# Kernel optimization log

Hardware: AMD Instinct MI355X
Metric: run time of the kernel (lower is better)

The kernel has to match this reference:

```python
import jax, jax.numpy as jnp
import numpy as np

TAU = 0.75

def normalize_W(W):
    n = jnp.linalg.norm(W)
    n = jax.nn.relu(n - 1.0) + 1.0
    return W / n

def setup_inputs() -> dict:
    key = jax.random.key(0)
    ks = jax.random.split(key, 14)
    C_in, C_out, K = 64, 128, 3
    B, L = 32, 4096
    nh = 64
    chunk_in_d = C_out * K            # 384
    D = C_in * (K + 2 * (C_out // C_in))  # 448
    r = lambda k, shp, s=1.0: jax.random.normal(k, shp, dtype=jnp.float32) * s
    W = normalize_W(r(ks[4], (D, 32)))
    return {
        "x": r(ks[0], (B, C_in, L)),
        "conv_weight": r(ks[1], (C_out, C_in, K), 0.1),
        "bias_param": r(ks[2], (C_out,), 0.1),
        "grads": r(ks[3], (C_out * C_in * K,), 0.1),
        "W": W,
        "ctrl_w": r(ks[5], (nh, chunk_in_d), 0.05),
        "ctrl_b": r(ks[6], (nh,), 0.05),
        "cw_w": r(ks[7], (K, nh), 0.05),
        "cw_b": r(ks[8], (K,), 0.05),
        "cb_w": r(ks[9], (C_out // C_in, nh), 0.05),
        "cb_b": r(ks[10], (C_out // C_in,), 0.05),
        "cf_w": r(ks[11], (C_out // C_in, nh), 0.05),
        "cf_b": r(ks[12], (C_out // C_in,), 0.05),
        "trigger": 1,
    }

def fw_chunks(grads, W, ctrl_w, ctrl_b, cw_w, cw_b, cb_w, cb_b, cf_w, cf_b, trigger, n_chunks):
    g = grads.reshape(n_chunks, -1)                    # (C_in, C_out*K)
    rep = jax.nn.silu(g @ ctrl_w.T + ctrl_b)           # (C_in, nh)
    w = rep @ cw_w.T + cw_b                            # (C_in, K)
    b = rep @ cb_w.T + cb_b                            # (C_in, C_out/C_in)
    f = rep @ cf_w.T + cf_b                            # (C_in, C_out/C_in)
    q = jnp.concatenate([w.ravel(), b.ravel(), f.ravel()])  # (D,)  first call: no q_ema
    W_upd = W
    if trigger == 1:  # codebook attention / top-k / scatter-EMA path
        dim = w.shape[0]
        att = jax.nn.softmax(q @ W / 0.5)              # (32,)
        v, idx = jax.lax.top_k(att, 2)
        ww = W[:, idx]                                 # (D, 2)
        old_w = ww @ idx.astype(jnp.float32)[:, None]  # (D, 1) -- indices used as weights, as in source
        s_att = jnp.zeros((att.shape[0],), jnp.float32).at[idx].set(v)
        W_contrib = old_w @ s_att[None, :]             # (D, 32)
        mask = jnp.ones(W.shape, jnp.float32).at[:, idx].set(TAU)
        W_upd = normalize_W(mask * W + (1.0 - mask) * W_contrib)
        nw, nb, nf = w.shape[1], b.shape[1], f.shape[1]
        o_w = old_w[: nw * dim]
        o_b = old_w[nw * dim : (nw + nb) * dim]
        o_f = old_w[-nf * dim :]
        w = TAU * w + (1.0 - TAU) * o_w.reshape(w.shape)
        b = TAU * b + (1.0 - TAU) * o_b.reshape(b.shape)
        f = TAU * f + (1.0 - TAU) * o_f.reshape(f.shape)
    f = f.reshape(-1)[None, :, None]                   # (1, C_out, 1)
    return w[None], b.reshape(-1), f, W_upd

def reference(x, conv_weight, bias_param, grads, W, ctrl_w, ctrl_b, cw_w, cw_b, cb_w, cb_b, cf_w, cf_b, trigger):
    n_chunks = conv_weight.shape[1]  # in_channels
    w, b, f, W_upd = fw_chunks(grads, W, ctrl_w, ctrl_b, cw_w, cw_b, cb_w, cb_b, cf_w, cf_b, trigger, n_chunks)
    cw = conv_weight * w                               # (C_out, C_in, K)
    pad = ((conv_weight.shape[2] - 1) * 1 + 1) // 2    # receptive_field // 2
    conv_out = jax.lax.conv_general_dilated(
        x, cw, window_strides=(1,), padding=[(pad, pad)], rhs_dilation=(1,),
        dimension_numbers=("NCH", "OIH", "NCH"))
    conv_out = conv_out + (bias_param * b)[None, :, None]
    out = f * conv_out                                 # (B, C_out, L)
    return out, W_upd
```

## Files before the change

kernel.cpp:

```cpp
#include <hip/hip_runtime.h>
#include <hip/hip_bf16.h>
#include <math.h>

#define TAU 0.75f

typedef _Float16 half8 __attribute__((ext_vector_type(8)));
typedef float    f32x4 __attribute__((ext_vector_type(4)));

#define SWZ(row) ((((row) >> 3) & 7) << 3)

#define WS_Q     0
#define WS_NORM2 448
#define WS_SCALE 449
#define WS_V01   450
#define WS_I01   452
#define WS_WQ    456
#define WS_FSC   648
#define WS_BADD  776
#define WS_OW    904
#define WS_WF16  1352

__global__ __launch_bounds__(256) void k1_rep_q(
    const float* __restrict__ grads, const float* __restrict__ ctrl_w,
    const float* __restrict__ ctrl_b,
    const float* __restrict__ cw_w, const float* __restrict__ cw_b,
    const float* __restrict__ cb_w, const float* __restrict__ cb_b,
    const float* __restrict__ cf_w, const float* __restrict__ cf_b,
    const float* __restrict__ W, float* __restrict__ ws)
{
    const int t = threadIdx.x;
    if (blockIdx.x == 64) {
        __shared__ float red[256];
        float ss = 0.f;
        for (int e = t; e < 3584; e += 256) {
            const float4 w4 = ((const float4*)W)[e];
            ss += w4.x * w4.x + w4.y * w4.y + w4.z * w4.z + w4.w * w4.w;
        }
        red[t] = ss; __syncthreads();
        for (int s = 128; s > 0; s >>= 1) { if (t < s) red[t] += red[t + s]; __syncthreads(); }
        if (t == 0) ws[WS_NORM2] = red[0];
        return;
    }
    const int c = blockIdx.x;
    __shared__ float gS[384];
    __shared__ float repS[64];
    if (t < 96) ((float4*)gS)[t] = ((const float4*)(grads + c * 384))[t];
    __syncthreads();
    {
        const int h = t >> 2, sub = t & 3;
        const float4* wa = (const float4*)(ctrl_w + h * 384) + sub * 24;
        const float4* ga = (const float4*)gS + sub * 24;
        float dot = 0.f;
        #pragma unroll
        for (int d = 0; d < 24; d++) {
            const float4 a = ga[d], b = wa[d];
            dot += a.x * b.x + a.y * b.y + a.z * b.z + a.w * b.w;
        }
        dot += __shfl_xor(dot, 1);
        dot += __shfl_xor(dot, 2);
        if (sub == 0) {
            const float z = dot + ctrl_b[h];
            repS[h] = z / (1.f + expf(-z));
        }
    }
    __syncthreads();
    if (t < 7) {
        const float* wv; float bias; int e;
        if (t < 3)      { wv = cw_w + t * 64;       bias = cw_b[t];     e = 3 * c + t; }
        else if (t < 5) { const int j = t - 3; wv = cb_w + j * 64; bias = cb_b[j]; e = 192 + 2 * c + j; }
        else            { const int j = t - 5; wv = cf_w + j * 64; bias = cf_b[j]; e = 320 + 2 * c + j; }
        float dot = 0.f;
        #pragma unroll 8
        for (int h = 0; h < 64; h++) dot += repS[h] * wv[h];
        ws[WS_Q + e] = dot + bias;
    }
}

__global__ __launch_bounds__(256) void k2_small(
    const float* __restrict__ W, const float* __restrict__ bias_param,
    const int* __restrict__ trigger, float* __restrict__ ws)
{
    __shared__ float qS[448], owS[448], sS[32], sW[4][32], red[256];
    __shared__ int   idxS[2];
    __shared__ float vS[2];
    const int t = threadIdx.x;
    const int wv = t >> 6, lane = t & 63;
    const int trig = trigger[0];

    for (int e = t; e < 448; e += 256) qS[e] = ws[WS_Q + e];
    __syncthreads();

    {
        const int m = lane & 31, half = lane >> 5;
        float s = 0.f;
        const int base = wv * 112;
        #pragma unroll 4
        for (int it = 0; it < 56; it++) {
            const int d = base + it * 2 + half;
            s += qS[d] * W[d * 32 + m];
        }
        s += __shfl_xor(s, 32);
        if (lane < 32) sW[wv][lane] = s;
    }
    __syncthreads();
    if (t < 32) sS[t] = 2.f * (sW[0][t] + sW[1][t] + sW[2][t] + sW[3][t]);
    __syncthreads();
    if (t == 0) {
        float mx = sS[0];
        for (int m = 1; m < 32; m++) mx = fmaxf(mx, sS[m]);
        float sum = 0.f; float att[32];
        for (int m = 0; m < 32; m++) { att[m] = expf(sS[m] - mx); sum += att[m]; }
        const float inv = 1.f / sum;
        int i0 = 0; float v0 = att[0];
        for (int m = 1; m < 32; m++) if (att[m] > v0) { v0 = att[m]; i0 = m; }
        int i1 = -1; float v1 = -1.f;
        for (int m = 0; m < 32; m++) { if (m == i0) continue; if (att[m] > v1) { v1 = att[m]; i1 = m; } }
        idxS[0] = i0; idxS[1] = i1; vS[0] = v0 * inv; vS[1] = v1 * inv;
    }
    __syncthreads();
    const int i0 = idxS[0], i1 = idxS[1];
    const float v0 = vS[0], v1 = vS[1];

    float corr = 0.f;
    for (int d = t; d < 448; d += 256) {
        const float w0 = W[d * 32 + i0], w1 = W[d * 32 + i1];
        const float ow = (trig == 1) ? (w0 * (float)i0 + w1 * (float)i1) : 0.f;
        owS[d] = ow;
        if (trig == 1) {
            const float n0 = TAU * w0 + 0.25f * ow * v0;
            const float n1 = TAU * w1 + 0.25f * ow * v1;
            corr += n0 * n0 - w0 * w0 + n1 * n1 - w1 * w1;
        }
    }
    red[t] = corr; __syncthreads();
    for (int s = 128; s > 0; s >>= 1) { if (t < s) red[t] += red[t + s]; __syncthreads(); }
    if (t == 0) {
        const float n = sqrtf(fmaxf(ws[WS_NORM2] + red[0], 0.f));
        ws[WS_SCALE] = 1.f / fmaxf(n, 1.f);
        ws[WS_V01] = v0; ws[WS_V01 + 1] = v1;
        ((int*)ws)[WS_I01] = i0; ((int*)ws)[WS_I01 + 1] = i1;
    }

    if (t < 192) ws[WS_WQ + t] = (trig == 1) ? (TAU * qS[t] + 0.25f * owS[t]) : qS[t];
    for (int o = t; o < 128; o += 256) {
        float bb = qS[192 + o], ff = qS[320 + o];
        if (trig == 1) {
            bb = TAU * bb + 0.25f * owS[192 + o];
            ff = TAU * ff + 0.25f * owS[320 + o];
        }
        ws[WS_FSC + o]  = ff;
        ws[WS_BADD + o] = ff * bias_param[o] * bb;
    }
    for (int d = t; d < 448; d += 256) ws[WS_OW + d] = owS[d];
}

__global__ __launch_bounds__(256) void k3_finalize(
    const float* __restrict__ W, const float* __restrict__ conv_weight,
    const int* __restrict__ trigger, const float* __restrict__ ws,
    float* __restrict__ W_out, _Float16* __restrict__ wf_out)
{
    const int g = blockIdx.x * 256 + threadIdx.x;
    const int trig = trigger[0];
    if (g < 14336) {
        const float wv = W[g];
        float wn = wv;
        if (trig == 1) {
            const int d = g >> 5, m = g & 31;
            const int i0 = ((const int*)ws)[WS_I01], i1 = ((const int*)ws)[WS_I01 + 1];
            if (m == i0)      wn = TAU * wv + 0.25f * ws[WS_OW + d] * ws[WS_V01];
            else if (m == i1) wn = TAU * wv + 0.25f * ws[WS_OW + d] * ws[WS_V01 + 1];
            wn *= ws[WS_SCALE];
        }
        W_out[g] = wn;
    } else {
        const int e2 = g - 14336;
        const int o   = e2 / 192;
        const int rem = e2 - o * 192;
        const int i   = rem / 3;
        const int kk  = rem - i * 3;
        wf_out[(kk * 128 + o) * 64 + i] =
            (_Float16)(conv_weight[e2] * ws[WS_WQ + rem] * ws[WS_FSC + o]);
    }
}

__global__ __launch_bounds__(256, 2) void conv_mfma(
    const float* __restrict__ x, const _Float16* __restrict__ wf,
    const float* __restrict__ badd, float* __restrict__ out)
{
    __shared__ __align__(16) _Float16 xs[4][66 * 72];

    const int t    = threadIdx.x;
    const int wv   = t >> 6;
    const int lane = t & 63;
    const int lrow = lane & 15;
    const int lgrp = lane >> 4;
    const int b    = blockIdx.x >> 4;
    const int lb   = (blockIdx.x & 15) * 256 + wv * 64;

    const float* xb = x + (size_t)b * 64 * 4096;
    _Float16* buf = xs[wv];

    {
        const int i = lane;
        const float* xr = xb + (size_t)i * 4096 + lb;
        #pragma unroll
        for (int j = 0; j < 16; j++) {
            const float4 v = *(const float4*)(xr + j * 4);
            const int c0 = j * 4 + 1;
            buf[(c0 + 0) * 72 + (i ^ SWZ(c0 + 0))] = (_Float16)v.x;
            buf[(c0 + 1) * 72 + (i ^ SWZ(c0 + 1))] = (_Float16)v.y;
            buf[(c0 + 2) * 72 + (i ^ SWZ(c0 + 2))] = (_Float16)v.z;
            buf[(c0 + 3) * 72 + (i ^ SWZ(c0 + 3))] = (_Float16)v.w;
        }
        float xl = 0.f, xh = 0.f;
        if (lb > 0)        xl = xr[-1];
        if (lb + 64 < 4096) xh = xr[64];
        buf[0 * 72 + (i ^ SWZ(0))]   = (_Float16)xl;
        buf[65 * 72 + (i ^ SWZ(65))] = (_Float16)xh;
    }

    f32x4 acc[8][4];
    #pragma unroll
    for (int of = 0; of < 8; of++)
        #pragma unroll
        for (int lf = 0; lf < 4; lf++) acc[of][lf] = (f32x4)0.f;

    #pragma unroll
    for (int ch = 0; ch < 2; ch++) {
        #pragma unroll
        for (int kk = 0; kk < 3; kk++) {
            half8 Xf[4];
            #pragma unroll
            for (int lf = 0; lf < 4; lf++) {
                const int rr = lf * 16 + lrow + kk;
                Xf[lf] = *(const half8*)(buf + rr * 72 + ((ch * 32 + lgrp * 8) ^ SWZ(rr)));
            }
            #pragma unroll
            for (int of = 0; of < 8; of++) {
                const half8 Wfv = *(const half8*)(wf +
                    ((kk * 128 + of * 16 + lrow) * 64 + ch * 32 + lgrp * 8));
                #pragma unroll
                for (int lf = 0; lf < 4; lf++)
                    acc[of][lf] = __builtin_amdgcn_mfma_f32_16x16x32_f16(Xf[lf], Wfv, acc[of][lf], 0, 0, 0);
            }
        }
    }

    #pragma unroll
    for (int of = 0; of < 8; of++) {
        const int o = of * 16 + lrow;
        const float ba = badd[o];
        float* orow = out + ((size_t)(b * 128 + o)) * 4096 + lb + lgrp * 4;
        #pragma unroll
        for (int lf = 0; lf < 4; lf++) {
            float4 r;
            r.x = acc[of][lf][0] + ba;
            r.y = acc[of][lf][1] + ba;
            r.z = acc[of][lf][2] + ba;
            r.w = acc[of][lf][3] + ba;
            *(float4*)(orow + lf * 16) = r;
        }
    }
}

extern "C" void kernel_launch(void* const* d_in, const int* in_sizes, int n_in,
                              void* d_out, int out_size, void* d_ws, size_t ws_size,
                              hipStream_t stream) {
    const float* x           = (const float*)d_in[0];
    const float* conv_weight = (const float*)d_in[1];
    const float* bias_param  = (const float*)d_in[2];
    const float* grads       = (const float*)d_in[3];
    const float* W           = (const float*)d_in[4];
    const float* ctrl_w      = (const float*)d_in[5];
    const float* ctrl_b      = (const float*)d_in[6];
    const float* cw_w        = (const float*)d_in[7];
    const float* cw_b        = (const float*)d_in[8];
    const float* cb_w        = (const float*)d_in[9];
    const float* cb_b        = (const float*)d_in[10];
    const float* cf_w        = (const float*)d_in[11];
    const float* cf_b        = (const float*)d_in[12];
    const int*   trigger     = (const int*)d_in[13];

    float* out   = (float*)d_out;
    float* W_out = out + (size_t)32 * 128 * 4096;
    float* ws    = (float*)d_ws;
    _Float16* wfp = (_Float16*)(ws + WS_WF16);
    float* badd  = ws + WS_BADD;

    k1_rep_q<<<65, 256, 0, stream>>>(grads, ctrl_w, ctrl_b, cw_w, cw_b,
                                     cb_w, cb_b, cf_w, cf_b, W, ws);
    k2_small<<<1, 256, 0, stream>>>(W, bias_param, trigger, ws);
    k3_finalize<<<152, 256, 0, stream>>>(W, conv_weight, trigger, ws, W_out, wfp);
    conv_mfma<<<512, 256, 0, stream>>>(x, wfp, badd, out);
}
```

Baseline: 50.18 us.

## Split conv output channels across waves and raise occupancy with smaller L tiles

The conv kernel now gives each block a 64-position tile. Each of its four waves computes 32 output channels instead of all 128 for its own 64 positions. The grid grows fourfold, and launch bounds now request four blocks per CU. Weights and bias are preloaded into registers, and all x loads are issued before the LDS stores, to cut register pressure and hide memory latency better. The cost is that each wave redundantly stages the same x tile into its own LDS buffer, so x is read four times per block, mostly from cache.

```diff
diff --git a/kernel.cpp b/kernel.cpp
--- a/kernel.cpp
+++ b/kernel.cpp
@@ -183,45 +183,73 @@
     }
 }
 
-__global__ __launch_bounds__(256, 2) void conv_mfma(
+__global__ __launch_bounds__(256, 4) void conv_mfma(
     const float* __restrict__ x, const _Float16* __restrict__ wf,
     const float* __restrict__ badd, float* __restrict__ out)
 {
     __shared__ __align__(16) _Float16 xs[4][66 * 72];
 
     const int t    = threadIdx.x;
-    const int wv   = t >> 6;
+    const int w    = t >> 6;
     const int lane = t & 63;
     const int lrow = lane & 15;
     const int lgrp = lane >> 4;
-    const int b    = blockIdx.x >> 4;
-    const int lb   = (blockIdx.x & 15) * 256 + wv * 64;
+    const int b    = blockIdx.x >> 6;
+    const int lt   = blockIdx.x & 63;
+    const int l0   = lt * 64;
+    const int obase = w * 32;
 
     const float* xb = x + (size_t)b * 64 * 4096;
-    _Float16* buf = xs[wv];
-
-    {
-        const int i = lane;
-        const float* xr = xb + (size_t)i * 4096 + lb;
-        #pragma unroll
-        for (int j = 0; j < 16; j++) {
-            const float4 v = *(const float4*)(xr + j * 4);
-            const int c0 = j * 4 + 1;
-            buf[(c0 + 0) * 72 + (i ^ SWZ(c0 + 0))] = (_Float16)v.x;
-            buf[(c0 + 1) * 72 + (i ^ SWZ(c0 + 1))] = (_Float16)v.y;
-            buf[(c0 + 2) * 72 + (i ^ SWZ(c0 + 2))] = (_Float16)v.z;
-            buf[(c0 + 3) * 72 + (i ^ SWZ(c0 + 3))] = (_Float16)v.w;
-        }
-        float xl = 0.f, xh = 0.f;
-        if (lb > 0)        xl = xr[-1];
-        if (lb + 64 < 4096) xh = xr[64];
-        buf[0 * 72 + (i ^ SWZ(0))]   = (_Float16)xl;
-        buf[65 * 72 + (i ^ SWZ(65))] = (_Float16)xh;
-    }
-
-    f32x4 acc[8][4];
-    #pragma unroll
-    for (int of = 0; of < 8; of++)
+    _Float16* buf = xs[w];
+
+    const int irr = lane >> 2;
+    const int ci  = lane & 3;
+
+    float4 v[4][4];
+    float  e0[4], e1[4];
+    #pragma unroll
+    for (int g = 0; g < 4; g++) {
+        const int i = g * 16 + irr;
+        const float* xr = xb + (size_t)i * 4096 + l0;
+        #pragma unroll
+        for (int j = 0; j < 4; j++)
+            v[g][j] = *(const float4*)(xr + j * 16 + ci * 4);
+        e0[g] = 0.f; e1[g] = 0.f;
+        if (ci == 0 && l0 > 0)         e0[g] = xr[-1];
+        if (ci == 3 && l0 + 64 < 4096) e1[g] = xr[64];
+    }
+    #pragma unroll
+    for (int g = 0; g < 4; g++) {
+        const int i = g * 16 + irr;
+        #pragma unroll
+        for (int j = 0; j < 4; j++) {
+            const int r0 = j * 16 + ci * 4 + 1;
+            buf[(r0 + 0) * 72 + (i ^ SWZ(r0 + 0))] = (_Float16)v[g][j].x;
+            buf[(r0 + 1) * 72 + (i ^ SWZ(r0 + 1))] = (_Float16)v[g][j].y;
+            buf[(r0 + 2) * 72 + (i ^ SWZ(r0 + 2))] = (_Float16)v[g][j].z;
+            buf[(r0 + 3) * 72 + (i ^ SWZ(r0 + 3))] = (_Float16)v[g][j].w;
+        }
+        if (ci == 0) buf[0 * 72  + (i ^ SWZ(0))]  = (_Float16)e0[g];
+        if (ci == 3) buf[65 * 72 + (i ^ SWZ(65))] = (_Float16)e1[g];
+    }
+
+    half8 Wf[2][2][3];
+    #pragma unroll
+    for (int of = 0; of < 2; of++)
+        #pragma unroll
+        for (int ch = 0; ch < 2; ch++)
+            #pragma unroll
+            for (int kk = 0; kk < 3; kk++)
+                Wf[of][ch][kk] = *(const half8*)(wf + ((kk * 128 + obase + of * 16 + lrow) * 64 + ch * 32 + lgrp * 8));
+
+    float ba_[2];
+    #pragma unroll
+    for (int of = 0; of < 2; of++)
+        ba_[of] = badd[obase + of * 16 + lrow];
+
+    f32x4 acc[2][4];
+    #pragma unroll
+    for (int of = 0; of < 2; of++)
         #pragma unroll
         for (int lf = 0; lf < 4; lf++) acc[of][lf] = (f32x4)0.f;
 
@@ -236,28 +264,24 @@
                 Xf[lf] = *(const half8*)(buf + rr * 72 + ((ch * 32 + lgrp * 8) ^ SWZ(rr)));
             }
             #pragma unroll
-            for (int of = 0; of < 8; of++) {
-                const half8 Wfv = *(const half8*)(wf +
-                    ((kk * 128 + of * 16 + lrow) * 64 + ch * 32 + lgrp * 8));
+            for (int of = 0; of < 2; of++)
                 #pragma unroll
                 for (int lf = 0; lf < 4; lf++)
-                    acc[of][lf] = __builtin_amdgcn_mfma_f32_16x16x32_f16(Xf[lf], Wfv, acc[of][lf], 0, 0, 0);
-            }
-        }
-    }
-
-    #pragma unroll
-    for (int of = 0; of < 8; of++) {
-        const int o = of * 16 + lrow;
-        const float ba = badd[o];
-        float* orow = out + ((size_t)(b * 128 + o)) * 4096 + lb + lgrp * 4;
+                    acc[of][lf] = __builtin_amdgcn_mfma_f32_16x16x32_f16(Xf[lf], Wf[of][ch][kk], acc[of][lf], 0, 0, 0);
+        }
+    }
+
+    #pragma unroll
+    for (int of = 0; of < 2; of++) {
+        const int o = obase + of * 16 + lrow;
+        float* orow = out + ((size_t)(b * 128 + o)) * 4096 + l0 + lgrp * 4;
         #pragma unroll
         for (int lf = 0; lf < 4; lf++) {
             float4 r;
-            r.x = acc[of][lf][0] + ba;
-            r.y = acc[of][lf][1] + ba;
-            r.z = acc[of][lf][2] + ba;
-            r.w = acc[of][lf][3] + ba;
+            r.x = acc[of][lf][0] + ba_[of];
+            r.y = acc[of][lf][1] + ba_[of];
+            r.z = acc[of][lf][2] + ba_[of];
+            r.w = acc[of][lf][3] + ba_[of];
             *(float4*)(orow + lf * 16) = r;
         }
     }
@@ -291,5 +315,5 @@
                                      cb_w, cb_b, cf_w, cf_b, W, ws);
     k2_small<<<1, 256, 0, stream>>>(W, bias_param, trigger, ws);
     k3_finalize<<<152, 256, 0, stream>>>(W, conv_weight, trigger, ws, W_out, wfp);
-    conv_mfma<<<512, 256, 0, stream>>>(x, wfp, badd, out);
-}
+    conv_mfma<<<2048, 256, 0, stream>>>(x, wfp, badd, out);
+}
```

New measurement: 54.77 us. +9.1%, slower.
